# Kernel tuning notes

Measured on AMD Instinct MI355X. Metric: run time of the kernel, lower is better.

Reference implementation:

```python
import jax, jax.numpy as jnp
import numpy as np


def setup_inputs() -> dict:
    key = jax.random.key(0)
    ks = jax.random.split(key, 11)
    d = 64
    inp = {
        "query_emb": jax.random.normal(ks[0], (d,), dtype=jnp.float32),
        "prog_embs": jax.random.normal(ks[1], (262144, d), dtype=jnp.float32),
        "stack_embs": jax.random.normal(ks[2], (131072, d), dtype=jnp.float32),
        "local_embs": jax.random.normal(ks[3], (131072, d), dtype=jnp.float32),
        "heap_embs": jax.random.normal(ks[4], (262144, d), dtype=jnp.float32),
        "call_embs": jax.random.normal(ks[5], (32768, d), dtype=jnp.float32),
        "WQ": jax.random.normal(ks[6], (10, 2, d), dtype=jnp.float32),
        "bQ": jax.random.normal(ks[7], (10, 2), dtype=jnp.float32),
        "WK": jax.random.normal(ks[8], (10, 2, d), dtype=jnp.float32),
        "WV1": jax.random.normal(ks[9], (9, 1, d), dtype=jnp.float32),
        "WV_call": jax.random.normal(ks[10], (1, 3, d), dtype=jnp.float32),
    }
    return inp


def _lookup(query_emb, mem, wq, bq, wk, wv):
    """Hard-max attention for a group of heads sharing one memory bank.
    wq/wk: [h,2,d], bq: [h,2], wv: [h,v,d], mem: [n,d]."""
    q = jnp.einsum('htd,d->ht', wq, query_emb) + bq          # [h,2]
    scores = jnp.einsum('htd,nd,ht->hn', wk, mem, q)         # K @ q per head
    best = jnp.argmax(scores, axis=1)                        # [h]
    best_scores = jnp.take_along_axis(scores, best[:, None], axis=1)[:, 0]
    vals = jnp.einsum('hvd,hd->hv', wv, mem[best])           # V[best] per head
    return vals, best_scores, best


def reference(query_emb, prog_embs, stack_embs, local_embs, heap_embs,
              call_embs, WQ, bQ, WK, WV1, WV_call):
    # head routing: 0-1 prog, 2-4 stack, 5-6 local, 7-8 heap, 9 call(v_dim=3)
    v_p, s_p, b_p = _lookup(query_emb, prog_embs,  WQ[0:2], bQ[0:2], WK[0:2], WV1[0:2])
    v_s, s_s, b_s = _lookup(query_emb, stack_embs, WQ[2:5], bQ[2:5], WK[2:5], WV1[2:5])
    v_l, s_l, b_l = _lookup(query_emb, local_embs, WQ[5:7], bQ[5:7], WK[5:7], WV1[5:7])
    v_h, s_h, b_h = _lookup(query_emb, heap_embs,  WQ[7:9], bQ[7:9], WK[7:9], WV1[7:9])
    v_c, s_c, b_c = _lookup(query_emb, call_embs,  WQ[9:10], bQ[9:10], WK[9:10], WV_call)
    values = jnp.concatenate([v_p.ravel(), v_s.ravel(), v_l.ravel(),
                              v_h.ravel(), v_c.ravel()])       # [12]
    best_scores = jnp.concatenate([s_p, s_s, s_l, s_h, s_c])   # [10]
    best_idx = jnp.concatenate([b_p, b_s, b_l, b_h, b_c])      # [10]
    return values, best_scores, best_idx
```

## Files before the change

kernel.cpp:

```cpp
#include <hip/hip_runtime.h>
#include <math.h>

#define PACK_OFF 640

__device__ __constant__ int HOFF[10] = {0, 1024, 2048, 2560, 3072, 3584, 4096, 4608, 5632, 6656};
__device__ __constant__ int HCNT[10] = {1024, 1024, 512, 512, 512, 512, 512, 1024, 1024, 128};

__device__ __forceinline__ unsigned int fkey(float f) {
  unsigned int u = __float_as_uint(f);
  return (u & 0x80000000u) ? ~u : (u | 0x80000000u);
}
__device__ __forceinline__ float funkey(unsigned int k) {
  unsigned int u = (k & 0x80000000u) ? (k & 0x7fffffffu) : ~k;
  return __uint_as_float(u);
}
__device__ __forceinline__ float dot4(float4 a, float4 b) {
  return a.x * b.x + a.y * b.y + a.z * b.z + a.w * b.w;
}

__global__ void prep_kernel(const float* __restrict__ query,
                            const float* __restrict__ WQ,
                            const float* __restrict__ bQ,
                            const float* __restrict__ WK,
                            float* __restrict__ ws) {
  __shared__ float q[20];
  int tid = threadIdx.x;
  if (tid < 20) {
    const float* w = WQ + tid * 64;
    float s = bQ[tid];
    for (int d = 0; d < 64; ++d) s += w[d] * query[d];
    q[tid] = s;
  }
  __syncthreads();
  for (int i = tid; i < 640; i += 256) {
    int h = i >> 6, d = i & 63;
    ws[i] = q[h * 2] * WK[h * 128 + d] + q[h * 2 + 1] * WK[h * 128 + 64 + d];
  }
}

__global__ __launch_bounds__(256) void scan_kernel(
    const float* __restrict__ prog, const float* __restrict__ stck,
    const float* __restrict__ locl, const float* __restrict__ heap,
    const float* __restrict__ call, float* __restrict__ ws) {
  const float* keff = ws;
  unsigned long long* res = (unsigned long long*)(ws + PACK_OFF);

  int b = blockIdx.x;
  const float* mem; int h0, nh, brank;
  int off0, off1, off2;
  if (b < 1024)      { mem = prog; h0 = 0; nh = 2; brank = b;
                       off0 = 0 + brank;    off1 = 1024 + brank; off2 = 0; }
  else if (b < 1536) { mem = stck; h0 = 2; nh = 3; brank = b - 1024;
                       off0 = 2048 + brank; off1 = 2560 + brank; off2 = 3072 + brank; }
  else if (b < 2048) { mem = locl; h0 = 5; nh = 2; brank = b - 1536;
                       off0 = 3584 + brank; off1 = 4096 + brank; off2 = 0; }
  else if (b < 3072) { mem = heap; h0 = 7; nh = 2; brank = b - 2048;
                       off0 = 4608 + brank; off1 = 5632 + brank; off2 = 0; }
  else               { mem = call; h0 = 9; nh = 1; brank = b - 3072;
                       off0 = 6656 + brank; off1 = 0;            off2 = 0; }

  int tid = threadIdx.x;
  int lane4 = tid & 3;
  int rsub = tid >> 2;

  float4 z = make_float4(0.f, 0.f, 0.f, 0.f);
  float4 ka[4], kb[4], kc[4];
#pragma unroll
  for (int j = 0; j < 4; ++j) {
    ka[j] = ((const float4*)(keff + (h0 + 0) * 64 + lane4 * 16))[j];
    kb[j] = (nh > 1) ? ((const float4*)(keff + (h0 + 1) * 64 + lane4 * 16))[j] : z;
    kc[j] = (nh > 2) ? ((const float4*)(keff + (h0 + 2) * 64 + lane4 * 16))[j] : z;
  }

  float bsA = -INFINITY, bsB = -INFINITY, bsC = -INFINITY;
  int biA = 0, biB = 0, biC = 0;

  int base = b < 3072 ? brank * 256 : brank * 256;
  base = brank * 256;
#pragma unroll 2
  for (int it = 0; it < 4; ++it) {
    int r = base + it * 64 + rsub;
    const float4* rowp = (const float4*)(mem + (size_t)r * 64 + lane4 * 16);
    float4 v0 = rowp[0];
    float4 v1 = rowp[1];
    float4 v2 = rowp[2];
    float4 v3 = rowp[3];

    float sA = dot4(v0, ka[0]) + dot4(v1, ka[1]) + dot4(v2, ka[2]) + dot4(v3, ka[3]);
    float sB = dot4(v0, kb[0]) + dot4(v1, kb[1]) + dot4(v2, kb[2]) + dot4(v3, kb[3]);
    float sC = dot4(v0, kc[0]) + dot4(v1, kc[1]) + dot4(v2, kc[2]) + dot4(v3, kc[3]);

    sA += __shfl_xor(sA, 1); sA += __shfl_xor(sA, 2);
    sB += __shfl_xor(sB, 1); sB += __shfl_xor(sB, 2);
    sC += __shfl_xor(sC, 1); sC += __shfl_xor(sC, 2);

    if (sA > bsA) { bsA = sA; biA = r; }
    if (sB > bsB) { bsB = sB; biB = r; }
    if (sC > bsC) { bsC = sC; biC = r; }
  }

  unsigned long long p0 = ((unsigned long long)fkey(bsA) << 32) | (unsigned long long)(0xFFFFFFFFu - (unsigned)biA);
  unsigned long long p1 = ((unsigned long long)fkey(bsB) << 32) | (unsigned long long)(0xFFFFFFFFu - (unsigned)biB);
  unsigned long long p2 = ((unsigned long long)fkey(bsC) << 32) | (unsigned long long)(0xFFFFFFFFu - (unsigned)biC);
#pragma unroll
  for (int m = 4; m < 64; m <<= 1) {
    unsigned long long t;
    t = __shfl_xor(p0, m); if (t > p0) p0 = t;
    t = __shfl_xor(p1, m); if (t > p1) p1 = t;
    t = __shfl_xor(p2, m); if (t > p2) p2 = t;
  }
  __shared__ unsigned long long red[3][4];
  int wv = tid >> 6;
  if ((tid & 63) == 0) { red[0][wv] = p0; red[1][wv] = p1; red[2][wv] = p2; }
  __syncthreads();
  if (tid == 0) {
    unsigned long long m0 = red[0][0], m1 = red[1][0], m2 = red[2][0];
#pragma unroll
    for (int w = 1; w < 4; ++w) {
      if (red[0][w] > m0) m0 = red[0][w];
      if (red[1][w] > m1) m1 = red[1][w];
      if (red[2][w] > m2) m2 = red[2][w];
    }
    res[off0] = m0;
    if (nh > 1) res[off1] = m1;
    if (nh > 2) res[off2] = m2;
  }
}

__global__ __launch_bounds__(640) void epi_kernel(
    const float* __restrict__ prog, const float* __restrict__ stck,
    const float* __restrict__ locl, const float* __restrict__ heap,
    const float* __restrict__ call,
    const float* __restrict__ WV1, const float* __restrict__ WVc,
    const float* __restrict__ ws, float* __restrict__ out) {
  const unsigned long long* res = (const unsigned long long*)(ws + PACK_OFF);
  __shared__ int sidx[10];
  int tid = threadIdx.x;
  int w = tid >> 6, lane = tid & 63;
  if (w < 10) {
    const unsigned long long* base = res + HOFF[w];
    int n = HCNT[w];
    unsigned long long m = 0ull;
    for (int i = lane; i < n; i += 64) {
      unsigned long long v = base[i];
      if (v > m) m = v;
    }
#pragma unroll
    for (int s = 1; s < 64; s <<= 1) {
      unsigned long long t = __shfl_xor(m, s);
      if (t > m) m = t;
    }
    if (lane == 0) {
      unsigned int key = (unsigned int)(m >> 32);
      int idx = (int)(0xFFFFFFFFu - (unsigned int)(m & 0xFFFFFFFFull));
      sidx[w] = idx;
      out[12 + w] = funkey(key);
      out[22 + w] = (float)idx;
    }
  }
  __syncthreads();
  int p = tid >> 4, l = tid & 15;
  if (p < 12) {
    int hh = (p < 9) ? p : 9;
    const float* wrow = (p < 9) ? (WV1 + p * 64) : (WVc + (p - 9) * 64);
    const float* mem;
    if (hh < 2) mem = prog;
    else if (hh < 5) mem = stck;
    else if (hh < 7) mem = locl;
    else if (hh < 9) mem = heap;
    else mem = call;
    const float* row = mem + (size_t)sidx[hh] * 64;
    float s = 0.f;
#pragma unroll
    for (int j = 0; j < 4; ++j) s += wrow[l * 4 + j] * row[l * 4 + j];
#pragma unroll
    for (int m = 1; m < 16; m <<= 1) s += __shfl_xor(s, m);
    if (l == 0) out[p] = s;
  }
}

extern "C" void kernel_launch(void* const* d_in, const int* in_sizes, int n_in,
                              void* d_out, int out_size, void* d_ws, size_t ws_size,
                              hipStream_t stream) {
  const float* query = (const float*)d_in[0];
  const float* prog  = (const float*)d_in[1];
  const float* stck  = (const float*)d_in[2];
  const float* locl  = (const float*)d_in[3];
  const float* heap  = (const float*)d_in[4];
  const float* call  = (const float*)d_in[5];
  const float* WQ    = (const float*)d_in[6];
  const float* bQ    = (const float*)d_in[7];
  const float* WK    = (const float*)d_in[8];
  const float* WV1   = (const float*)d_in[9];
  const float* WVc   = (const float*)d_in[10];
  float* ws  = (float*)d_ws;
  float* out = (float*)d_out;

  hipLaunchKernelGGL(prep_kernel, dim3(1), dim3(256), 0, stream, query, WQ, bQ, WK, ws);
  hipLaunchKernelGGL(scan_kernel, dim3(3200), dim3(256), 0, stream,
                     prog, stck, locl, heap, call, ws);
  hipLaunchKernelGGL(epi_kernel, dim3(1), dim3(640), 0, stream,
                     prog, stck, locl, heap, call, WV1, WVc, ws, out);
}
```

Baseline: 48.59 us.

## Fuse query projection into scan kernel and double rows per block

Removes the separate prep kernel: each scan block now computes its heads' query projection and effective key vector into shared memory before scanning. The grid is halved so each block scans 512 rows, and the per-lane loads are interleaved across the row for better coalescing. This saves a kernel launch and the dependency on a workspace round trip, at the cost of redundant per-block projection work and a serial prologue.

```diff
diff --git a/kernel.cpp b/kernel.cpp
--- a/kernel.cpp
+++ b/kernel.cpp
@@ -1,90 +1,81 @@
 #include <hip/hip_runtime.h>
 #include <math.h>
 
-#define PACK_OFF 640
+__device__ __constant__ int HOFF[10] = {0, 512, 1024, 1280, 1536, 1792, 2048, 2304, 2816, 3328};
+__device__ __constant__ int HCNT[10] = {512, 512, 256, 256, 256, 256, 256, 512, 512, 64};
 
-__device__ __constant__ int HOFF[10] = {0, 1024, 2048, 2560, 3072, 3584, 4096, 4608, 5632, 6656};
-__device__ __constant__ int HCNT[10] = {1024, 1024, 512, 512, 512, 512, 512, 1024, 1024, 128};
-
-__device__ __forceinline__ unsigned int fkey(float f) {
+static __device__ __forceinline__ unsigned int fkey(float f) {
   unsigned int u = __float_as_uint(f);
   return (u & 0x80000000u) ? ~u : (u | 0x80000000u);
 }
-__device__ __forceinline__ float funkey(unsigned int k) {
+static __device__ __forceinline__ float funkey(unsigned int k) {
   unsigned int u = (k & 0x80000000u) ? (k & 0x7fffffffu) : ~k;
   return __uint_as_float(u);
 }
-__device__ __forceinline__ float dot4(float4 a, float4 b) {
+static __device__ __forceinline__ float dot4(float4 a, float4 b) {
   return a.x * b.x + a.y * b.y + a.z * b.z + a.w * b.w;
 }
 
-__global__ void prep_kernel(const float* __restrict__ query,
-                            const float* __restrict__ WQ,
-                            const float* __restrict__ bQ,
-                            const float* __restrict__ WK,
-                            float* __restrict__ ws) {
-  __shared__ float q[20];
-  int tid = threadIdx.x;
-  if (tid < 20) {
-    const float* w = WQ + tid * 64;
-    float s = bQ[tid];
-    for (int d = 0; d < 64; ++d) s += w[d] * query[d];
-    q[tid] = s;
+__global__ __launch_bounds__(256) void scan_kernel(
+    const float* __restrict__ query,
+    const float* __restrict__ prog, const float* __restrict__ stck,
+    const float* __restrict__ locl, const float* __restrict__ heap,
+    const float* __restrict__ call,
+    const float* __restrict__ WQ, const float* __restrict__ bQ,
+    const float* __restrict__ WK, float* __restrict__ ws)
+{
+  unsigned long long* res = (unsigned long long*)ws;
+  int b = blockIdx.x, tid = threadIdx.x;
+
+  const float* mem; int h0, nh, brank, off0, off1, off2;
+  if (b < 512)       { mem = prog; h0 = 0; nh = 2; brank = b;        off0 = 0    + brank; off1 = 512  + brank; off2 = 0; }
+  else if (b < 768)  { mem = stck; h0 = 2; nh = 3; brank = b - 512;  off0 = 1024 + brank; off1 = 1280 + brank; off2 = 1536 + brank; }
+  else if (b < 1024) { mem = locl; h0 = 5; nh = 2; brank = b - 768;  off0 = 1792 + brank; off1 = 2048 + brank; off2 = 0; }
+  else if (b < 1536) { mem = heap; h0 = 7; nh = 2; brank = b - 1024; off0 = 2304 + brank; off1 = 2816 + brank; off2 = 0; }
+  else               { mem = call; h0 = 9; nh = 1; brank = b - 1536; off0 = 3328 + brank; off1 = 0;            off2 = 0; }
+
+  __shared__ float qs[6];
+  __shared__ float skeff[3][64];
+  if (tid < 2 * nh) {
+    int t = tid;
+    const float* wq = WQ + (h0 * 2 + t) * 64;
+    float s = bQ[h0 * 2 + t];
+    for (int d = 0; d < 64; ++d) s += wq[d] * query[d];
+    qs[t] = s;
   }
   __syncthreads();
-  for (int i = tid; i < 640; i += 256) {
-    int h = i >> 6, d = i & 63;
-    ws[i] = q[h * 2] * WK[h * 128 + d] + q[h * 2 + 1] * WK[h * 128 + 64 + d];
+  if (tid < 192) {
+    int i = tid >> 6, d = tid & 63;
+    float v = 0.f;
+    if (i < nh) {
+      int h = h0 + i;
+      v = qs[2 * i] * WK[(h * 2) * 64 + d] + qs[2 * i + 1] * WK[(h * 2 + 1) * 64 + d];
+    }
+    skeff[i][d] = v;
   }
-}
+  __syncthreads();
 
-__global__ __launch_bounds__(256) void scan_kernel(
-    const float* __restrict__ prog, const float* __restrict__ stck,
-    const float* __restrict__ locl, const float* __restrict__ heap,
-    const float* __restrict__ call, float* __restrict__ ws) {
-  const float* keff = ws;
-  unsigned long long* res = (unsigned long long*)(ws + PACK_OFF);
+  int lane4 = tid & 3, rsub = tid >> 2;
 
-  int b = blockIdx.x;
-  const float* mem; int h0, nh, brank;
-  int off0, off1, off2;
-  if (b < 1024)      { mem = prog; h0 = 0; nh = 2; brank = b;
-                       off0 = 0 + brank;    off1 = 1024 + brank; off2 = 0; }
-  else if (b < 1536) { mem = stck; h0 = 2; nh = 3; brank = b - 1024;
-                       off0 = 2048 + brank; off1 = 2560 + brank; off2 = 3072 + brank; }
-  else if (b < 2048) { mem = locl; h0 = 5; nh = 2; brank = b - 1536;
-                       off0 = 3584 + brank; off1 = 4096 + brank; off2 = 0; }
-  else if (b < 3072) { mem = heap; h0 = 7; nh = 2; brank = b - 2048;
-                       off0 = 4608 + brank; off1 = 5632 + brank; off2 = 0; }
-  else               { mem = call; h0 = 9; nh = 1; brank = b - 3072;
-                       off0 = 6656 + brank; off1 = 0;            off2 = 0; }
-
-  int tid = threadIdx.x;
-  int lane4 = tid & 3;
-  int rsub = tid >> 2;
-
-  float4 z = make_float4(0.f, 0.f, 0.f, 0.f);
   float4 ka[4], kb[4], kc[4];
 #pragma unroll
   for (int j = 0; j < 4; ++j) {
-    ka[j] = ((const float4*)(keff + (h0 + 0) * 64 + lane4 * 16))[j];
-    kb[j] = (nh > 1) ? ((const float4*)(keff + (h0 + 1) * 64 + lane4 * 16))[j] : z;
-    kc[j] = (nh > 2) ? ((const float4*)(keff + (h0 + 2) * 64 + lane4 * 16))[j] : z;
+    ka[j] = ((const float4*)skeff[0])[j * 4 + lane4];
+    kb[j] = ((const float4*)skeff[1])[j * 4 + lane4];
+    kc[j] = ((const float4*)skeff[2])[j * 4 + lane4];
   }
 
   float bsA = -INFINITY, bsB = -INFINITY, bsC = -INFINITY;
   int biA = 0, biB = 0, biC = 0;
-
-  int base = b < 3072 ? brank * 256 : brank * 256;
-  base = brank * 256;
+  int base = brank * 512;
 #pragma unroll 2
-  for (int it = 0; it < 4; ++it) {
+  for (int it = 0; it < 8; ++it) {
     int r = base + it * 64 + rsub;
-    const float4* rowp = (const float4*)(mem + (size_t)r * 64 + lane4 * 16);
-    float4 v0 = rowp[0];
-    float4 v1 = rowp[1];
-    float4 v2 = rowp[2];
-    float4 v3 = rowp[3];
+    const float* rowp = mem + (size_t)r * 64 + lane4 * 4;
+    float4 v0 = *(const float4*)(rowp +  0);
+    float4 v1 = *(const float4*)(rowp + 16);
+    float4 v2 = *(const float4*)(rowp + 32);
+    float4 v3 = *(const float4*)(rowp + 48);
 
     float sA = dot4(v0, ka[0]) + dot4(v1, ka[1]) + dot4(v2, ka[2]) + dot4(v3, ka[3]);
     float sB = dot4(v0, kb[0]) + dot4(v1, kb[1]) + dot4(v2, kb[2]) + dot4(v3, kb[3]);
@@ -133,16 +124,16 @@
     const float* __restrict__ call,
     const float* __restrict__ WV1, const float* __restrict__ WVc,
     const float* __restrict__ ws, float* __restrict__ out) {
-  const unsigned long long* res = (const unsigned long long*)(ws + PACK_OFF);
+  const unsigned long long* res = (const unsigned long long*)ws;
   __shared__ int sidx[10];
   int tid = threadIdx.x;
   int w = tid >> 6, lane = tid & 63;
   if (w < 10) {
-    const unsigned long long* base = res + HOFF[w];
+    const unsigned long long* basep = res + HOFF[w];
     int n = HCNT[w];
     unsigned long long m = 0ull;
     for (int i = lane; i < n; i += 64) {
-      unsigned long long v = base[i];
+      unsigned long long v = basep[i];
       if (v > m) m = v;
     }
 #pragma unroll
@@ -163,18 +154,18 @@
   if (p < 12) {
     int hh = (p < 9) ? p : 9;
     const float* wrow = (p < 9) ? (WV1 + p * 64) : (WVc + (p - 9) * 64);
-    const float* mem;
-    if (hh < 2) mem = prog;
-    else if (hh < 5) mem = stck;
-    else if (hh < 7) mem = locl;
-    else if (hh < 9) mem = heap;
-    else mem = call;
-    const float* row = mem + (size_t)sidx[hh] * 64;
+    const float* vmem;
+    if (hh < 2) vmem = prog;
+    else if (hh < 5) vmem = stck;
+    else if (hh < 7) vmem = locl;
+    else if (hh < 9) vmem = heap;
+    else vmem = call;
+    const float* row = vmem + (size_t)sidx[hh] * 64;
     float s = 0.f;
 #pragma unroll
     for (int j = 0; j < 4; ++j) s += wrow[l * 4 + j] * row[l * 4 + j];
 #pragma unroll
-    for (int m = 1; m < 16; m <<= 1) s += __shfl_xor(s, m);
+    for (int m2 = 1; m2 < 16; m2 <<= 1) s += __shfl_xor(s, m2);
     if (l == 0) out[p] = s;
   }
 }
@@ -196,9 +187,8 @@
   float* ws  = (float*)d_ws;
   float* out = (float*)d_out;
 
-  hipLaunchKernelGGL(prep_kernel, dim3(1), dim3(256), 0, stream, query, WQ, bQ, WK, ws);
-  hipLaunchKernelGGL(scan_kernel, dim3(3200), dim3(256), 0, stream,
-                     prog, stck, locl, heap, call, ws);
+  hipLaunchKernelGGL(scan_kernel, dim3(1600), dim3(256), 0, stream,
+                     query, prog, stck, locl, heap, call, WQ, bQ, WK, ws);
   hipLaunchKernelGGL(epi_kernel, dim3(1), dim3(640), 0, stream,
                      prog, stck, locl, heap, call, WV1, WVc, ws, out);
 }
```

Result: faster. 47.33 us (-2.6%).
